# Kernel tuning notes

Hardware: AMD Instinct MI355X
Metric: run time of the kernel (lower is better)

## Reference

```python
import jax, jax.numpy as jnp
import numpy as np

B, S, L, D, M = 32, 256, 64, 100, 20  # batch, n_sentences, max_sentence_len, embed_dim, n_memories


def setup_inputs() -> dict:
    key = jax.random.key(0)
    ks = jax.random.split(key, 6)
    batch = jax.random.normal(ks[0], (B, S, L, D), dtype=jnp.float32)
    enc_mult = jnp.ones((L, D), dtype=jnp.float32)  # input_encoder_multiplier (init to ones)
    keys = 0.1 * jax.random.normal(ks[1], (M, D), dtype=jnp.float32)
    U = 0.1 * jax.random.normal(ks[2], (D, D), dtype=jnp.float32)  # nn.Linear weight [out,in]
    V = 0.1 * jax.random.normal(ks[3], (D, D), dtype=jnp.float32)
    W = 0.1 * jax.random.normal(ks[4], (D, D), dtype=jnp.float32)
    prelu_a = jnp.ones((), dtype=jnp.float32)  # PReLU(init=1), single shared parameter
    return {"batch": batch, "enc_mult": enc_mult, "keys": keys, "U": U, "V": V, "W": W, "prelu_a": prelu_a}


def reference(batch, enc_mult, keys, U, V, W, prelu_a):
    # Encode: elementwise multiply by learned positional multiplier, sum over words -> [B, S, D]
    enc = (batch * enc_mult).sum(axis=2)

    def prelu(x):
        return jnp.where(x >= 0, x, prelu_a * x)

    # keys @ V.T is step-invariant
    keysV = jnp.einsum('md,ed->me', keys, V)  # [M, D]

    def step(mem, s):  # mem: [B, M, D], s: [B, D]
        memory_gate = jnp.einsum('bd,bmd->bm', s, mem)          # [B, M]
        key_gate = jnp.einsum('bd,md->bm', s, keys)              # [B, M]
        gate = jax.nn.sigmoid(memory_gate + key_gate)            # [B, M]
        cand = prelu(
            jnp.einsum('bmd,ed->bme', mem, U)                    # U(memories)
            + keysV[None, :, :]                                  # V(keys)
            + jnp.einsum('bd,ed->be', s, W)[:, None, :]          # W(sentence), broadcast over M
        )
        mem = mem + cand * gate[:, :, None]
        mem = mem / jnp.linalg.norm(mem, axis=2, keepdims=True)  # L2 normalize each memory slot
        return mem, None

    mem0 = jnp.broadcast_to(keys[None, :, :], (B, M, D))  # memories init = keys repeated per batch
    mem_final, _ = jax.lax.scan(step, mem0, jnp.swapaxes(enc, 0, 1))  # scan over sentences
    return mem_final
```

## Files before the change

### kernel.cpp

```cpp
#include <hip/hip_runtime.h>


typedef float v2f __attribute__((ext_vector_type(2)));

__global__ __launch_bounds__(320) void encode_k(
    const float* __restrict__ batch,
    const float* __restrict__ encm,
    float* __restrict__ enc)
{
    __shared__ float prod[6400];
    __shared__ float part[200];
    const int t = threadIdx.x;
    const int row = blockIdx.x;
    const float4* rb = (const float4*)batch + (size_t)row * 1600;
    const float4* e4 = (const float4*)encm;
    float4* p4 = (float4*)prod;
    #pragma unroll
    for (int i = 0; i < 5; ++i) {
        const int idx = i * 320 + t;
        float4 x = rb[idx];
        float4 mu = e4[idx];
        float4 p;
        p.x = x.x * mu.x; p.y = x.y * mu.y; p.z = x.z * mu.z; p.w = x.w * mu.w;
        p4[idx] = p;
    }
    __syncthreads();
    if (t < 200) {
        const int c = (t < 100) ? t : (t - 100);
        const int l0 = (t < 100) ? 0 : 32;
        float s0 = 0.f, s1 = 0.f;
        #pragma unroll
        for (int l = 0; l < 32; l += 2) {
            s0 += prod[(l0 + l) * 100 + c];
            s1 += prod[(l0 + l + 1) * 100 + c];
        }
        part[t] = s0 + s1;
    }
    __syncthreads();
    if (t < 100) enc[(size_t)row * 100 + t] = part[t] + part[100 + t];
}

__global__ void prep_k(const float* __restrict__ W,
                       const float* __restrict__ keys,
                       float* __restrict__ T)
{
    const int d = blockIdx.x;
    const int e = threadIdx.x;
    float v = 0.f;
    if (e < 100) v = W[e * 100 + d];
    else if (e < 120) v = keys[(e - 100) * 100 + d];
    T[d * 128 + e] = v;
}

__global__ __launch_bounds__(128) void project_k(
    const float* __restrict__ enc,
    const float* __restrict__ T,
    float* __restrict__ sWp,
    float* __restrict__ kg)
{
    __shared__ float encS[400];
    const int t = threadIdx.x;
    const int row0 = blockIdx.x * 4;
    if (t < 100) ((float4*)encS)[t] = ((const float4*)(enc + (size_t)row0 * 100))[t];
    __syncthreads();
    float a0 = 0.f, a1 = 0.f, a2 = 0.f, a3 = 0.f;
    #pragma unroll 4
    for (int d = 0; d < 100; ++d) {
        const float w = T[d * 128 + t];
        a0 += w * encS[d];
        a1 += w * encS[100 + d];
        a2 += w * encS[200 + d];
        a3 += w * encS[300 + d];
    }
    if (t < 100) {
        sWp[(size_t)row0 * 100 + t]       = a0;
        sWp[(size_t)(row0 + 1) * 100 + t] = a1;
        sWp[(size_t)(row0 + 2) * 100 + t] = a2;
        sWp[(size_t)(row0 + 3) * 100 + t] = a3;
    } else if (t < 120) {
        const int m = t - 100;
        kg[(size_t)row0 * 20 + m]       = a0;
        kg[(size_t)(row0 + 1) * 20 + m] = a1;
        kg[(size_t)(row0 + 2) * 20 + m] = a2;
        kg[(size_t)(row0 + 3) * 20 + m] = a3;
    }
}

template <int CTRL>
__device__ __forceinline__ float dpp_add_f(float x) {
    int s = __builtin_amdgcn_update_dpp(0, __float_as_int(x), CTRL, 0xF, 0xF, true);
    return x + __int_as_float(s);
}
__device__ __forceinline__ float lane63(float x) {
    return __int_as_float(__builtin_amdgcn_readlane(__float_as_int(x), 63));
}
#define DPP6(v) v = dpp_add_f<0x111>(v); v = dpp_add_f<0x112>(v); v = dpp_add_f<0x114>(v); \
                v = dpp_add_f<0x118>(v); v = dpp_add_f<0x142>(v); v = dpp_add_f<0x143>(v);

#define MATVEC100(RES, SRC4)                                                   \
    {                                                                          \
        v2f A0 = {0.f,0.f}, A1 = {0.f,0.f}, A2 = {0.f,0.f}, A3 = {0.f,0.f};    \
        _Pragma("unroll")                                                      \
        for (int k = 0; k < 25; ++k) {                                         \
            float4 v = (SRC4)[k];                                              \
            A0 += Upk[4 * k + 0] * v.x;                                        \
            A1 += Upk[4 * k + 1] * v.y;                                        \
            A2 += Upk[4 * k + 2] * v.z;                                        \
            A3 += Upk[4 * k + 3] * v.w;                                        \
        }                                                                      \
        RES = (A0 + A1) + (A2 + A3);                                           \
    }

__global__ __attribute__((amdgpu_waves_per_eu(1, 1))) __launch_bounds__(64)
void entnet_scan(
    const float* __restrict__ enc,
    const float* __restrict__ sWp,
    const float* __restrict__ kg,
    const float* __restrict__ keys,
    const float* __restrict__ U,
    const float* __restrict__ V,
    const float* __restrict__ paPtr,
    float* __restrict__ out)
{
    __shared__ float4 cand4[32];
    float* candF = (float*)cand4;
    const int lane = threadIdx.x;
    const int b = blockIdx.x / 20;
    const int m = blockIdx.x % 20;
    const bool hi = (lane < 36);
    const float h = hi ? 1.f : 0.f;
    const int e0 = lane;
    const int e1 = hi ? (64 + lane) : 99;
    const float pa = paPtr[0];

    v2f Upk[100];
    {
        const float4* u0 = (const float4*)(U + e0 * 100);
        const float4* u1 = (const float4*)(U + e1 * 100);
        #pragma unroll
        for (int k = 0; k < 25; ++k) {
            float4 a = u0[k], c = u1[k];
            Upk[4 * k + 0] = (v2f){a.x, c.x};
            Upk[4 * k + 1] = (v2f){a.y, c.y};
            Upk[4 * k + 2] = (v2f){a.z, c.z};
            Upk[4 * k + 3] = (v2f){a.w, c.w};
        }
    }
    float kv0 = 0.f, kv1 = 0.f;
    {
        const float4* km = (const float4*)(keys + m * 100);
        const float4* v0 = (const float4*)(V + e0 * 100);
        const float4* v1 = (const float4*)(V + e1 * 100);
        #pragma unroll
        for (int k = 0; k < 25; ++k) {
            float4 kk = km[k], a = v0[k], c = v1[k];
            kv0 += a.x * kk.x + a.y * kk.y + a.z * kk.z + a.w * kk.w;
            kv1 += c.x * kk.x + c.y * kk.y + c.z * kk.z + c.w * kk.w;
        }
    }
    const float k0 = keys[m * 100 + e0];
    const float k1 = h * keys[m * 100 + e1];
    float nm0 = k0, nm1 = k1;
    candF[lane] = nm0;
    candF[64 + lane] = nm1;
    __asm__ __volatile__("" ::: "memory");

    v2f P;
    MATVEC100(P, cand4);

    float nq = k0 * k0 + k1 * k1;
    DPP6(nq)
    float nsq = lane63(nq);
    float rn = 1.f;

    const float* encRow = enc + (size_t)b * 25600;
    const float* sWRow  = sWp + (size_t)b * 25600;
    const float* kgRow  = kg + (size_t)b * 5120 + m;

    float sw0 = sWRow[e0], sw1 = sWRow[e1];
    float g;
    {
        const float sv0 = encRow[e0], sv1 = encRow[e1];
        const float kg0 = kgRow[0];
        float q1 = sv0 * nm0 + sv1 * nm1;
        DPP6(q1)
        const float Q1 = lane63(q1);
        g = 1.f / (1.f + __expf(-(Q1 + kg0)));
    }

    for (int step = 0; step < 256; ++step) {
        const int nxt = (step < 255 ? step + 1 : 255);
        const float nsv0 = encRow[nxt * 100 + e0], nsv1 = encRow[nxt * 100 + e1];
        const float nsw0 = sWRow[nxt * 100 + e0], nsw1 = sWRow[nxt * 100 + e1];
        const float nkg  = kgRow[nxt * 20];

        const float x0 = rn * P.x + kv0 + sw0;
        const float x1 = rn * P.y + kv1 + sw1;
        float c0 = (x0 >= 0.f) ? x0 : pa * x0;
        float c1 = (x1 >= 0.f) ? x1 : pa * x1;
        c1 *= h;
        candF[lane] = c0;
        candF[64 + lane] = c1;
        __asm__ __volatile__("" ::: "memory");

        float q3 = nm0 * c0 + nm1 * c1;
        float p4 = c0 * c0 + c1 * c1;
        #define RND2(C) q3 = dpp_add_f<C>(q3); p4 = dpp_add_f<C>(p4);
        RND2(0x111) RND2(0x112) RND2(0x114) RND2(0x118) RND2(0x142) RND2(0x143)
        #undef RND2

        v2f Q;
        MATVEC100(Q, cand4);

        const float Q3 = lane63(q3);
        const float P4 = lane63(p4);
        const float n2 = nsq + 2.f * (g * rn) * Q3 + g * g * P4;
        const float rnn = rsqrtf(n2);
        nsq = 1.f;

        nm0 = rn * nm0 + g * c0;
        nm1 = rn * nm1 + g * c1;
        P = rn * P + g * Q;

        float q1 = nsv0 * nm0 + nsv1 * nm1;
        DPP6(q1)
        const float Q1 = lane63(q1);
        g = 1.f / (1.f + __expf(-(rnn * Q1 + nkg)));

        rn = rnn;
        sw0 = nsw0; sw1 = nsw1;
    }
    const float* dummy = V;  (void)dummy;
    float* orow = out + (size_t)(b * 20 + m) * 100;
    orow[e0] = nm0 * rn;
    if (hi) orow[e1] = nm1 * rn;
}

extern "C" void kernel_launch(void* const* d_in, const int* in_sizes, int n_in,
                              void* d_out, int out_size, void* d_ws, size_t ws_size,
                              hipStream_t stream) {
    const float* batch = (const float*)d_in[0];
    const float* encm  = (const float*)d_in[1];
    const float* keys  = (const float*)d_in[2];
    const float* U     = (const float*)d_in[3];
    const float* V     = (const float*)d_in[4];
    const float* W     = (const float*)d_in[5];
    const float* pa    = (const float*)d_in[6];
    float* out = (float*)d_out;

    float* enc = (float*)d_ws;
    float* sWp = enc + 819200;
    float* kgb = sWp + 819200;
    float* T   = kgb + 163840;

    encode_k<<<8192, 320, 0, stream>>>(batch, encm, enc);
    prep_k<<<100, 128, 0, stream>>>(W, keys, T);
    project_k<<<2048, 128, 0, stream>>>(enc, T, sWp, kgb);
    entnet_scan<<<640, 64, 0, stream>>>(enc, sWp, kgb, keys, U, V, pa, out);
}
```

Before: 515.6 us.

## Replace LDS matvec broadcast with readlane scalar broadcasts and XCD-aware block mapping

The per-step 100x100 matvec no longer writes the candidate vector to shared memory and reads it back as float4. Each element is instead broadcast from its owning lane with v_readlane into an SGPR and used in scalar FMAs against per-lane U rows. The block index is also remapped so the four batches handled by each XCD are grouped together. This removes LDS round-trip latency from the serial scan's critical path, but adds 100 readlane instructions per matvec and changes v2f packed math to scalar FMAs.

```diff
diff --git a/kernel.cpp b/kernel.cpp
--- a/kernel.cpp
+++ b/kernel.cpp
@@ -94,20 +94,20 @@
 __device__ __forceinline__ float lane63(float x) {
     return __int_as_float(__builtin_amdgcn_readlane(__float_as_int(x), 63));
 }
+template <int L>
+__device__ __forceinline__ float bcast(float x) {
+    return __int_as_float(__builtin_amdgcn_readlane(__float_as_int(x), L));
+}
 #define DPP6(v) v = dpp_add_f<0x111>(v); v = dpp_add_f<0x112>(v); v = dpp_add_f<0x114>(v); \
                 v = dpp_add_f<0x118>(v); v = dpp_add_f<0x142>(v); v = dpp_add_f<0x143>(v);
 
-#define MATVEC100(RES, SRC4)                                                   \
+#define MVSTEP(A, k, ck) { float c_ = (ck); A.x = __builtin_fmaf(U0[k], c_, A.x); \
+                                            A.y = __builtin_fmaf(U1[k], c_, A.y); }
+#define MATVECRL(RES, S0, S1)                                                  \
     {                                                                          \
         v2f A0 = {0.f,0.f}, A1 = {0.f,0.f}, A2 = {0.f,0.f}, A3 = {0.f,0.f};    \
-        _Pragma("unroll")                                                      \
-        for (int k = 0; k < 25; ++k) {                                         \
-            float4 v = (SRC4)[k];                                              \
-            A0 += Upk[4 * k + 0] * v.x;                                        \
-            A1 += Upk[4 * k + 1] * v.y;                                        \
-            A2 += Upk[4 * k + 2] * v.z;                                        \
-            A3 += Upk[4 * k + 3] * v.w;                                        \
-        }                                                                      \
+        mv_unroll64(A0, A1, A2, A3, S0);                                       \
+        mv_unroll36(A0, A1, A2, A3, S1);                                       \
         RES = (A0 + A1) + (A2 + A3);                                           \
     }
 
@@ -122,30 +122,48 @@
     const float* __restrict__ paPtr,
     float* __restrict__ out)
 {
-    __shared__ float4 cand4[32];
-    float* candF = (float*)cand4;
     const int lane = threadIdx.x;
-    const int b = blockIdx.x / 20;
-    const int m = blockIdx.x % 20;
+    const int xcd = blockIdx.x & 7;
+    const int gg  = blockIdx.x >> 3;
+    const int b = xcd * 4 + gg / 20;
+    const int m = gg % 20;
     const bool hi = (lane < 36);
     const float h = hi ? 1.f : 0.f;
     const int e0 = lane;
     const int e1 = hi ? (64 + lane) : 99;
     const float pa = paPtr[0];
 
-    v2f Upk[100];
+    float U0[100], U1[100];
     {
         const float4* u0 = (const float4*)(U + e0 * 100);
         const float4* u1 = (const float4*)(U + e1 * 100);
         #pragma unroll
         for (int k = 0; k < 25; ++k) {
             float4 a = u0[k], c = u1[k];
-            Upk[4 * k + 0] = (v2f){a.x, c.x};
-            Upk[4 * k + 1] = (v2f){a.y, c.y};
-            Upk[4 * k + 2] = (v2f){a.z, c.z};
-            Upk[4 * k + 3] = (v2f){a.w, c.w};
+            U0[4*k] = a.x; U0[4*k+1] = a.y; U0[4*k+2] = a.z; U0[4*k+3] = a.w;
+            U1[4*k] = c.x; U1[4*k+1] = c.y; U1[4*k+2] = c.z; U1[4*k+3] = c.w;
         }
     }
+    auto mv_unroll64 = [&](v2f& A0, v2f& A1, v2f& A2, v2f& A3, float S0) {
+        #define Q4(base) MVSTEP(A0, base+0, bcast<base+0>(S0)) \
+                         MVSTEP(A1, base+1, bcast<base+1>(S0)) \
+                         MVSTEP(A2, base+2, bcast<base+2>(S0)) \
+                         MVSTEP(A3, base+3, bcast<base+3>(S0))
+        Q4(0) Q4(4) Q4(8) Q4(12) Q4(16) Q4(20) Q4(24) Q4(28)
+        Q4(32) Q4(36) Q4(40) Q4(44) Q4(48) Q4(52) Q4(56) Q4(60)
+        #undef Q4
+    };
+    auto mv_unroll36 = [&](v2f& A0, v2f& A1, v2f& A2, v2f& A3, float S1) {
+        #define Q4(base) MVSTEP(A0, 64+base+0, bcast<base+0>(S1)) \
+                         MVSTEP(A1, 64+base+1, bcast<base+1>(S1)) \
+                         MVSTEP(A2, 64+base+2, bcast<base+2>(S1)) \
+                         MVSTEP(A3, 64+base+3, bcast<base+3>(S1))
+        Q4(0) Q4(4) Q4(8) Q4(12) Q4(16) Q4(20) Q4(24) Q4(28)
+        MVSTEP(A0, 96, bcast<32>(S1)) MVSTEP(A1, 97, bcast<33>(S1))
+        MVSTEP(A2, 98, bcast<34>(S1)) MVSTEP(A3, 99, bcast<35>(S1))
+        #undef Q4
+    };
+
     float kv0 = 0.f, kv1 = 0.f;
     {
         const float4* km = (const float4*)(keys + m * 100);
@@ -161,12 +179,9 @@
     const float k0 = keys[m * 100 + e0];
     const float k1 = h * keys[m * 100 + e1];
     float nm0 = k0, nm1 = k1;
-    candF[lane] = nm0;
-    candF[64 + lane] = nm1;
-    __asm__ __volatile__("" ::: "memory");
 
     v2f P;
-    MATVEC100(P, cand4);
+    MATVECRL(P, nm0, nm1);
 
     float nq = k0 * k0 + k1 * k1;
     DPP6(nq)
@@ -199,9 +214,6 @@
         float c0 = (x0 >= 0.f) ? x0 : pa * x0;
         float c1 = (x1 >= 0.f) ? x1 : pa * x1;
         c1 *= h;
-        candF[lane] = c0;
-        candF[64 + lane] = c1;
-        __asm__ __volatile__("" ::: "memory");
 
         float q3 = nm0 * c0 + nm1 * c1;
         float p4 = c0 * c0 + c1 * c1;
@@ -210,7 +222,7 @@
         #undef RND2
 
         v2f Q;
-        MATVEC100(Q, cand4);
+        MATVECRL(Q, c0, c1);
 
         const float Q3 = lane63(q3);
         const float P4 = lane63(p4);
@@ -230,7 +242,6 @@
         rn = rnn;
         sw0 = nsw0; sw1 = nsw1;
     }
-    const float* dummy = V;  (void)dummy;
     float* orow = out + (size_t)(b * 20 + m) * 100;
     orow[e0] = nm0 * rn;
     if (hi) orow[e1] = nm1 * rn;
```

Measured after the change: 512.1 us. No clear change (-0.7%).
